# Kernel tuning notes

Measured on AMD Instinct MI355X. Metric: run time of the kernel, lower is better.

Reference implementation:

```python
import jax, jax.numpy as jnp
import numpy as np

K = 64  # numOnBits

def setup_inputs() -> dict:
    key = jax.random.key(0)
    x = jax.random.normal(key, (8192, 16384), dtype=jnp.float32)
    return {"x": x}

def reference(x) -> jnp.ndarray:
    # Row-wise k-th largest value as threshold, then mask-multiply.
    rows = x.shape[0]
    tmpx = x.reshape(rows, -1)
    topvals, _ = jax.lax.top_k(tmpx, K)        # [rows, K]
    thresh = topvals[:, -1].reshape(rows, *([1] * (x.ndim - 1)))  # k-th largest per row
    comp = (x >= thresh).astype(x.dtype)
    return comp * x
```

## Files before the change

### kernel.cpp

```cpp
#include <hip/hip_runtime.h>

#define ROWLEN 16384
#define NF4 (ROWLEN / 4)
#define KSEL 64u

__device__ __forceinline__ unsigned f2k(float f) {
    unsigned u = __float_as_uint(f);
    return (u & 0x80000000u) ? ~u : (u | 0x80000000u);
}
__device__ __forceinline__ float k2f(unsigned k) {
    unsigned u = (k & 0x80000000u) ? (k ^ 0x80000000u) : ~k;
    return __uint_as_float(u);
}

__global__ __launch_bounds__(256, 4)
void sparsify_topk_kernel(const float* __restrict__ x, float* __restrict__ out, int rows) {
    const int t = threadIdx.x;
    const int row = blockIdx.x;
    if (row >= rows) return;

    __shared__ unsigned hist[256];
    __shared__ unsigned selBin, selK;

    const float4* xrow = (const float4*)(x + (size_t)row * ROWLEN);
    unsigned keys[64];
#pragma unroll
    for (int j = 0; j < 16; ++j) {
        float4 v = xrow[j * 256 + t];
        keys[4 * j + 0] = f2k(v.x);
        keys[4 * j + 1] = f2k(v.y);
        keys[4 * j + 2] = f2k(v.z);
        keys[4 * j + 3] = f2k(v.w);
    }

    unsigned prefix = 0;
    unsigned kcur = KSEL;

#define HPASS(SHIFT, FIRST)                                                    \
    {                                                                          \
        hist[t] = 0;                                                           \
        __syncthreads();                                                       \
        _Pragma("unroll")                                                      \
        for (int e = 0; e < 64; ++e) {                                         \
            unsigned key = keys[e];                                            \
            bool valid = (FIRST) || ((key >> ((SHIFT) + 8)) == prefix);        \
            if (valid) {                                                       \
                unsigned b = (key >> (SHIFT)) & 255u;                          \
                if (hist[b] < KSEL) atomicAdd(&hist[b], 1u);                   \
            }                                                                  \
        }                                                                      \
        __syncthreads();                                                       \
        if (t < 64) {                                                          \
            unsigned c0 = hist[4 * t + 0], c1 = hist[4 * t + 1];               \
            unsigned c2 = hist[4 * t + 2], c3 = hist[4 * t + 3];               \
            unsigned s = c0 + c1 + c2 + c3;                                    \
            _Pragma("unroll")                                                  \
            for (int d = 1; d < 64; d <<= 1) {                                 \
                unsigned v = __shfl_down(s, d);                                \
                if (t + d < 64) s += v;                                        \
            }                                                                  \
            unsigned sAb = __shfl_down(s, 1);                                  \
            if (t == 63) sAb = 0;                                              \
            if (s >= kcur && sAb < kcur) {               \
                unsigned a = sAb;                                              \
                int bin; unsigned kn;                                          \
                if (a + c3 >= kcur)                { bin = 4*t+3; kn = kcur - a; }                    \
                else if (a + c3 + c2 >= kcur)      { bin = 4*t+2; kn = kcur - a - c3; }               \
                else if (a + c3 + c2 + c1 >= kcur) { bin = 4*t+1; kn = kcur - a - c3 - c2; }          \
                else                               { bin = 4*t+0; kn = kcur - a - c3 - c2 - c1; }     \
                selBin = (unsigned)bin;                                        \
                selK = kn;                                                     \
            }                                                                  \
        }                                                                      \
        __syncthreads();                                                       \
        prefix = (prefix << 8) | selBin;                                       \
        kcur = selK;                                                           \
    }

    HPASS(24, true)
    HPASS(16, false)
    HPASS(8, false)
    HPASS(0, false)
#undef HPASS

    const unsigned tkey = prefix;

    float4* orow = (float4*)out + (size_t)row * NF4;
#pragma unroll
    for (int j = 0; j < 16; ++j) {
        unsigned k0 = keys[4 * j + 0], k1 = keys[4 * j + 1];
        unsigned k2 = keys[4 * j + 2], k3 = keys[4 * j + 3];
        float4 o;
        o.x = (k0 >= tkey) ? k2f(k0) : 0.0f;
        o.y = (k1 >= tkey) ? k2f(k1) : 0.0f;
        o.z = (k2 >= tkey) ? k2f(k2) : 0.0f;
        o.w = (k3 >= tkey) ? k2f(k3) : 0.0f;
        orow[j * 256 + t] = o;
    }
}

extern "C" void kernel_launch(void* const* d_in, const int* in_sizes, int n_in,
                              void* d_out, int out_size, void* d_ws, size_t ws_size,
                              hipStream_t stream) {
    const float* x = (const float*)d_in[0];
    float* out = (float*)d_out;
    const int rows = in_sizes[0] / ROWLEN;
    sparsify_topk_kernel<<<rows, 256, 0, stream>>>(x, out, rows);
}
```

Before: 853.0 us.

## Use 512 threads per row, double-buffer histograms, batch histogram reads

Doubles the block size to 512 threads so each thread keeps 32 keys in registers instead of 64, which lowers register pressure and raises occupancy. The histogram is now double-buffered: the idle upper threads clear the next pass's histogram during the scan, which removes one barrier per pass. The capped-atomic check is batched in groups of 8 so the LDS reads can overlap before the atomics are issued. The cost is more threads contending for the same LDS bins, and the cap on counts becomes looser because reads and atomics are separated.

```diff
diff --git a/kernel.cpp b/kernel.cpp
--- a/kernel.cpp
+++ b/kernel.cpp
@@ -2,6 +2,8 @@
 
 #define ROWLEN 16384
 #define NF4 (ROWLEN / 4)
+#define NT 512
+#define EPT 32
 #define KSEL 64u
 
 __device__ __forceinline__ unsigned f2k(float f) {
@@ -13,46 +15,54 @@
     return __uint_as_float(u);
 }
 
-__global__ __launch_bounds__(256, 4)
+__global__ __launch_bounds__(NT, 4)
 void sparsify_topk_kernel(const float* __restrict__ x, float* __restrict__ out, int rows) {
     const int t = threadIdx.x;
     const int row = blockIdx.x;
     if (row >= rows) return;
 
-    __shared__ unsigned hist[256];
+    __shared__ unsigned h0[256], h1[256];
     __shared__ unsigned selBin, selK;
 
     const float4* xrow = (const float4*)(x + (size_t)row * ROWLEN);
-    unsigned keys[64];
+    unsigned keys[EPT];
 #pragma unroll
-    for (int j = 0; j < 16; ++j) {
-        float4 v = xrow[j * 256 + t];
+    for (int j = 0; j < EPT / 4; ++j) {
+        float4 v = xrow[j * NT + t];
         keys[4 * j + 0] = f2k(v.x);
         keys[4 * j + 1] = f2k(v.y);
         keys[4 * j + 2] = f2k(v.z);
         keys[4 * j + 3] = f2k(v.w);
     }
 
+    if (t < 256) h0[t] = 0u;
+    else         h1[t - 256] = 0u;
+    __syncthreads();
+
     unsigned prefix = 0;
     unsigned kcur = KSEL;
 
-#define HPASS(SHIFT, FIRST)                                                    \
+#define HPASS(SHIFT, FIRST, HC, HN, ZN)                                        \
     {                                                                          \
-        hist[t] = 0;                                                           \
-        __syncthreads();                                                       \
         _Pragma("unroll")                                                      \
-        for (int e = 0; e < 64; ++e) {                                         \
-            unsigned key = keys[e];                                            \
-            bool valid = (FIRST) || ((key >> ((SHIFT) + 8)) == prefix);        \
-            if (valid) {                                                       \
-                unsigned b = (key >> (SHIFT)) & 255u;                          \
-                if (hist[b] < KSEL) atomicAdd(&hist[b], 1u);                   \
+        for (int g = 0; g < EPT; g += 8) {                                     \
+            unsigned bb[8], cc[8]; bool vl[8];                                 \
+            _Pragma("unroll")                                                  \
+            for (int i = 0; i < 8; ++i) {                                      \
+                unsigned key = keys[g + i];                                    \
+                vl[i] = (FIRST) || ((key >> ((SHIFT) + 8)) == prefix);         \
+                bb[i] = (key >> (SHIFT)) & 255u;                               \
             }                                                                  \
+            _Pragma("unroll")                                                  \
+            for (int i = 0; i < 8; ++i) cc[i] = vl[i] ? HC[bb[i]] : KSEL;      \
+            _Pragma("unroll")                                                  \
+            for (int i = 0; i < 8; ++i)                                        \
+                if (cc[i] < KSEL) atomicAdd(&HC[bb[i]], 1u);                   \
         }                                                                      \
         __syncthreads();                                                       \
         if (t < 64) {                                                          \
-            unsigned c0 = hist[4 * t + 0], c1 = hist[4 * t + 1];               \
-            unsigned c2 = hist[4 * t + 2], c3 = hist[4 * t + 3];               \
+            unsigned c0 = HC[4 * t + 0], c1 = HC[4 * t + 1];                   \
+            unsigned c2 = HC[4 * t + 2], c3 = HC[4 * t + 3];                   \
             unsigned s = c0 + c1 + c2 + c3;                                    \
             _Pragma("unroll")                                                  \
             for (int d = 1; d < 64; d <<= 1) {                                 \
@@ -71,23 +81,25 @@
                 selBin = (unsigned)bin;                                        \
                 selK = kn;                                                     \
             }                                                                  \
+        } else if ((ZN) && t >= 256) {                                         \
+            HN[t - 256] = 0u;      \
         }                                                                      \
         __syncthreads();                                                       \
         prefix = (prefix << 8) | selBin;                                       \
         kcur = selK;                                                           \
     }
 
-    HPASS(24, true)
-    HPASS(16, false)
-    HPASS(8, false)
-    HPASS(0, false)
+    HPASS(24, true,  h0, h1, 1)
+    HPASS(16, false, h1, h0, 1)
+    HPASS(8,  false, h0, h1, 1)
+    HPASS(0,  false, h1, h0, 0)
 #undef HPASS
 
     const unsigned tkey = prefix;
 
     float4* orow = (float4*)out + (size_t)row * NF4;
 #pragma unroll
-    for (int j = 0; j < 16; ++j) {
+    for (int j = 0; j < EPT / 4; ++j) {
         unsigned k0 = keys[4 * j + 0], k1 = keys[4 * j + 1];
         unsigned k2 = keys[4 * j + 2], k3 = keys[4 * j + 3];
         float4 o;
@@ -95,7 +107,7 @@
         o.y = (k1 >= tkey) ? k2f(k1) : 0.0f;
         o.z = (k2 >= tkey) ? k2f(k2) : 0.0f;
         o.w = (k3 >= tkey) ? k2f(k3) : 0.0f;
-        orow[j * 256 + t] = o;
+        orow[j * NT + t] = o;
     }
 }
 
@@ -105,5 +117,5 @@
     const float* x = (const float*)d_in[0];
     float* out = (float*)d_out;
     const int rows = in_sizes[0] / ROWLEN;
-    sparsify_topk_kernel<<<rows, 256, 0, stream>>>(x, out, rows);
+    sparsify_topk_kernel<<<rows, NT, 0, stream>>>(x, out, rows);
 }
```

Result: no change. 857.7 us (+0.6%).
